# Optimization experiments

Measured on AMD Instinct MI355X. Metric: run time of the kernel, lower is better.

## Reference

```python
import jax, jax.numpy as jnp
import numpy as np

N, E, IN, HID, Z, H = 10000, 320000, 128, 128, 64, 4


def setup_inputs() -> dict:
    key = jax.random.key(0)
    ks = jax.random.split(key, 24)
    s = 0.05
    inp = {
        "x": jax.random.normal(ks[0], (N, IN), jnp.float32),
        "edge_index": jax.random.randint(ks[1], (2, E), 0, N, jnp.int32),
        "eps": jax.random.normal(ks[2], (N, Z), jnp.float32),
        # GCNConv params
        "gcn_w": jax.random.normal(ks[3], (IN, HID), jnp.float32) * s,
        "gcn_b": jnp.zeros((HID,), jnp.float32),
        # GATConv params (heads=H, out=HID per head, concat=False)
        "gat_w": jax.random.normal(ks[4], (HID, H * HID), jnp.float32) * s,
        "gat_att_src": jax.random.normal(ks[5], (H, HID), jnp.float32) * s,
        "gat_att_dst": jax.random.normal(ks[6], (H, HID), jnp.float32) * s,
        "gat_b": jnp.zeros((HID,), jnp.float32),
        # encoder MLP
        "mlp_w1": jax.random.normal(ks[7], (HID, HID), jnp.float32) * s,
        "mlp_b1": jnp.zeros((HID,), jnp.float32),
        "mlp_w2": jax.random.normal(ks[8], (HID, HID), jnp.float32) * s,
        "mlp_b2": jnp.zeros((HID,), jnp.float32),
        "mu_w": jax.random.normal(ks[9], (HID, Z), jnp.float32) * s,
        "mu_b": jnp.zeros((Z,), jnp.float32),
        "lv_w": jax.random.normal(ks[10], (HID, Z), jnp.float32) * s,
        "lv_b": jnp.zeros((Z,), jnp.float32),
        # decoder
        "dec_w1": jax.random.normal(ks[11], (Z, HID), jnp.float32) * s,
        "dec_b1": jnp.zeros((HID,), jnp.float32),
        "dec_w2": jax.random.normal(ks[12], (HID, Z), jnp.float32) * s,
        "dec_b2": jnp.zeros((Z,), jnp.float32),
    }
    return inp


def _forward(x, eps, gcn_w, gcn_b, gat_w, gat_att_src, gat_att_dst, gat_b,
             mlp_w1, mlp_b1, mlp_w2, mlp_b2, mu_w, mu_b, lv_w, lv_b,
             dec_w1, dec_b1, dec_w2, dec_b2, src, dst):
    n = x.shape[0]
    # ---- GCNConv (symmetric norm, self loops already in src/dst) ----
    h = x @ gcn_w  # [N, HID]
    deg = jax.ops.segment_sum(jnp.ones_like(dst, jnp.float32), dst, num_segments=n)
    dinv = jnp.where(deg > 0, deg ** -0.5, 0.0)
    msg = h[src] * (dinv[src] * dinv[dst])[:, None]  # [E', HID]
    h = jax.nn.relu(jax.ops.segment_sum(msg, dst, num_segments=n) + gcn_b)
    # ---- GATConv (heads=H, concat=False -> mean over heads) ----
    g = (h @ gat_w).reshape(n, H, HID)  # [N,H,D]
    a_src = jnp.einsum("nhd,hd->nh", g, gat_att_src)  # [N,H]
    a_dst = jnp.einsum("nhd,hd->nh", g, gat_att_dst)
    e = jax.nn.leaky_relu(a_src[src] + a_dst[dst], 0.2)  # [E',H]
    emax = jax.ops.segment_max(e, dst, num_segments=n)
    ex = jnp.exp(e - emax[dst])
    den = jax.ops.segment_sum(ex, dst, num_segments=n)
    alpha = ex / den[dst]  # softmax over incoming edges
    agg = jax.ops.segment_sum(alpha[:, :, None] * g[src], dst, num_segments=n)
    h = jax.nn.relu(agg.mean(axis=1) + gat_b)  # [N,HID]
    # ---- MLP ----
    h = jax.nn.relu(h @ mlp_w1 + mlp_b1)
    h = jax.nn.relu(h @ mlp_w2 + mlp_b2)
    mu = h @ mu_w + mu_b
    logvar = h @ lv_w + lv_b
    # ---- reparameterize ----
    lv = jnp.clip(logvar, -10.0, 10.0)
    z = mu + eps * jnp.exp(0.5 * lv)
    # ---- decoder ----
    d = jax.nn.relu(z @ dec_w1 + dec_b1)
    d = d @ dec_w2 + dec_b2 + z
    logits = d @ d.T  # [N,N]
    return logits, mu, logvar


def reference(x, edge_index, eps, gcn_w, gcn_b, gat_w, gat_att_src, gat_att_dst,
              gat_b, mlp_w1, mlp_b1, mlp_w2, mlp_b2, mu_w, mu_b, lv_w, lv_b,
              dec_w1, dec_b1, dec_w2, dec_b2):
    n = x.shape[0]
    loop = jnp.arange(n, dtype=edge_index.dtype)
    src = jnp.concatenate([edge_index[0], loop])
    dst = jnp.concatenate([edge_index[1], loop])
    return _forward(x, eps, gcn_w, gcn_b, gat_w, gat_att_src, gat_att_dst,
                    gat_b, mlp_w1, mlp_b1, mlp_w2, mlp_b2, mu_w, mu_b,
                    lv_w, lv_b, dec_w1, dec_b1, dec_w2, dec_b2, src, dst)
```

## Files before the change

kernel.cpp:

```cpp
#include <hip/hip_runtime.h>
#include <hip/hip_bf16.h>

typedef unsigned short u16;
typedef unsigned int u32;

#define NN 10000
#define EE 320000

typedef __attribute__((ext_vector_type(8))) short short8;
typedef __attribute__((ext_vector_type(4))) float f32x4;

__device__ __forceinline__ u16 f2bfu(float f) {
    u32 x = __float_as_uint(f);
    x += 0x7FFFu + ((x >> 16) & 1u);
    return (u16)(x >> 16);
}
__device__ __forceinline__ float bfu2f(u16 u) { return __uint_as_float(((u32)u) << 16); }
__device__ __forceinline__ void ld4f(const float* p, float* o) {
    float4 v = *(const float4*)p; o[0] = v.x; o[1] = v.y; o[2] = v.z; o[3] = v.w;
}

__global__ void k_hist(const int* __restrict__ dst, int* __restrict__ cnt) {
    int e = blockIdx.x * 256 + threadIdx.x;
    if (e < EE) atomicAdd(&cnt[dst[e]], 1);
}

__global__ void k_dinv(const int* __restrict__ cnt, float* __restrict__ dinv) {
    int n = blockIdx.x * 256 + threadIdx.x;
    if (n < NN) dinv[n] = 1.f / sqrtf((float)(cnt[n] + 1));
}

__global__ void k_scan(const int* __restrict__ cnt, int* __restrict__ rowptr) {
    __shared__ int sh[1024];
    int t = threadIdx.x;
    int base = t * 10;
    int loc[10];
    int s = 0;
    #pragma unroll
    for (int i = 0; i < 10; i++) {
        int idx = base + i;
        int v = (idx < NN) ? cnt[idx] : 0;
        loc[i] = s; s += v;
    }
    sh[t] = s;
    __syncthreads();
    for (int off = 1; off < 1024; off <<= 1) {
        int v = (t >= off) ? sh[t - off] : 0;
        __syncthreads();
        sh[t] += v;
        __syncthreads();
    }
    int ex = sh[t] - s;
    #pragma unroll
    for (int i = 0; i < 10; i++) {
        int idx = base + i;
        if (idx < NN) rowptr[idx] = ex + loc[i];
    }
    if (t == 0) rowptr[NN] = EE;
}

__global__ void k_scatter(const int* __restrict__ src, const int* __restrict__ dst,
                          const int* __restrict__ rowptr, int* __restrict__ fill,
                          int* __restrict__ csr) {
    int e = blockIdx.x * 256 + threadIdx.x;
    if (e < EE) {
        int d = dst[e];
        int pos = rowptr[d] + atomicAdd(&fill[d], 1);
        csr[pos] = src[e];
    }
}

template <int K, int M, bool RELU, bool BIAS, bool OB16>
__global__ __launch_bounds__(256) void k_linear(const float* __restrict__ A, const float* __restrict__ W,
                                                const float* __restrict__ Bb, void* __restrict__ outv) {
    constexpr int MC = M / 64;
    int wid = (blockIdx.x * blockDim.x + threadIdx.x) >> 6;
    int lane = threadIdx.x & 63;
    int row0 = wid * 4;
    if (row0 >= NN) return;
    float acc[4][MC];
    #pragma unroll
    for (int i = 0; i < 4; i++)
        #pragma unroll
        for (int j = 0; j < MC; j++) acc[i][j] = 0.f;
    for (int k = 0; k < K; k += 4) {
        float a[4][4];
        #pragma unroll
        for (int i = 0; i < 4; i++) ld4f(A + (size_t)(row0 + i) * K + k, a[i]);
        #pragma unroll
        for (int kk = 0; kk < 4; kk++) {
            float wv[MC];
            #pragma unroll
            for (int j = 0; j < MC; j++) wv[j] = W[(size_t)(k + kk) * M + j * 64 + lane];
            #pragma unroll
            for (int i = 0; i < 4; i++)
                #pragma unroll
                for (int j = 0; j < MC; j++) acc[i][j] += a[i][kk] * wv[j];
        }
    }
    float* outf = (float*)outv;
    u16*   outb = (u16*)outv;
    #pragma unroll
    for (int i = 0; i < 4; i++) {
        int r = row0 + i;
        #pragma unroll
        for (int j = 0; j < MC; j++) {
            float v = acc[i][j];
            if constexpr (BIAS) v += Bb[j * 64 + lane];
            if constexpr (RELU) v = fmaxf(v, 0.f);
            if constexpr (OB16) outb[(size_t)r * M + j * 64 + lane] = f2bfu(v);
            else                outf[(size_t)r * M + j * 64 + lane] = v;
        }
    }
}

__global__ __launch_bounds__(256) void k_gcn_agg(const u16* __restrict__ h0, const int* __restrict__ rowptr,
                                                 const int* __restrict__ csr, const float* __restrict__ dinv,
                                                 const float* __restrict__ bias, float* __restrict__ h1) {
    int node = (blockIdx.x * blockDim.x + threadIdx.x) >> 6;
    int lane = threadIdx.x & 63;
    if (node >= NN) return;
    float di = dinv[node];
    u32 sv = *(const u32*)(h0 + (size_t)node * 128 + lane * 2);
    float acc0 = bfu2f((u16)(sv & 0xffffu)) * di * di;
    float acc1 = bfu2f((u16)(sv >> 16)) * di * di;
    int st = rowptr[node], en = rowptr[node + 1];
    for (int p = st; p < en; p++) {
        int s = csr[p];
        float w = dinv[s] * di;
        u32 gv = *(const u32*)(h0 + (size_t)s * 128 + lane * 2);
        acc0 += bfu2f((u16)(gv & 0xffffu)) * w;
        acc1 += bfu2f((u16)(gv >> 16)) * w;
    }
    acc0 = fmaxf(acc0 + bias[lane * 2], 0.f);
    acc1 = fmaxf(acc1 + bias[lane * 2 + 1], 0.f);
    float2 o; o.x = acc0; o.y = acc1;
    *(float2*)(h1 + (size_t)node * 128 + lane * 2) = o;
}

__global__ __launch_bounds__(256) void k_gat_linear(const float* __restrict__ A, const float* __restrict__ W,
                                                    const float* __restrict__ att_s, const float* __restrict__ att_d,
                                                    u16* __restrict__ gbf, float* __restrict__ a_src,
                                                    float* __restrict__ a_dst) {
    int wid = (blockIdx.x * blockDim.x + threadIdx.x) >> 6;
    int lane = threadIdx.x & 63;
    int row0 = wid * 4;
    if (row0 >= NN) return;
    float acc[4][8];
    #pragma unroll
    for (int i = 0; i < 4; i++)
        #pragma unroll
        for (int t = 0; t < 8; t++) acc[i][t] = 0.f;
    for (int k = 0; k < 128; k += 4) {
        float a[4][4];
        #pragma unroll
        for (int i = 0; i < 4; i++) ld4f(A + (size_t)(row0 + i) * 128 + k, a[i]);
        #pragma unroll
        for (int kk = 0; kk < 4; kk++) {
            float wv[8];
            ld4f(W + (size_t)(k + kk) * 512 + lane * 8, wv);
            ld4f(W + (size_t)(k + kk) * 512 + lane * 8 + 4, wv + 4);
            #pragma unroll
            for (int i = 0; i < 4; i++)
                #pragma unroll
                for (int t = 0; t < 8; t++) acc[i][t] += a[i][kk] * wv[t];
        }
    }
    float sv[8], dv[8];
    ld4f(att_s + lane * 8, sv); ld4f(att_s + lane * 8 + 4, sv + 4);
    ld4f(att_d + lane * 8, dv); ld4f(att_d + lane * 8 + 4, dv + 4);
    int head = lane >> 4;
    #pragma unroll
    for (int i = 0; i < 4; i++) {
        int r = row0 + i;
        short8 pk;
        #pragma unroll
        for (int t = 0; t < 8; t++) pk[t] = (short)f2bfu(acc[i][t]);
        *(short8*)(gbf + (size_t)r * 512 + lane * 8) = pk;
        float ps = 0.f, pd = 0.f;
        #pragma unroll
        for (int t = 0; t < 8; t++) { ps += acc[i][t] * sv[t]; pd += acc[i][t] * dv[t]; }
        #pragma unroll
        for (int off = 1; off < 16; off <<= 1) {
            ps += __shfl_xor(ps, off, 64);
            pd += __shfl_xor(pd, off, 64);
        }
        if ((lane & 15) == i) {
            a_src[r * 4 + head] = ps;
            a_dst[r * 4 + head] = pd;
        }
    }
}

__global__ __launch_bounds__(256) void k_gat_softmax(const int* __restrict__ rowptr, const int* __restrict__ csr,
                                                     const float* __restrict__ a_src, const float* __restrict__ a_dst,
                                                     float* __restrict__ alpha, float* __restrict__ selfalpha) {
    int node = (blockIdx.x * blockDim.x + threadIdx.x) >> 6;
    int lane = threadIdx.x & 63;
    if (node >= NN) return;
    float ad[4], asn[4];
    ld4f(a_dst + node * 4, ad);
    ld4f(a_src + node * 4, asn);
    float es[4], m[4];
    #pragma unroll
    for (int h = 0; h < 4; h++) {
        float e = asn[h] + ad[h];
        es[h] = e > 0.f ? e : 0.2f * e;
        m[h] = es[h];
    }
    int st = rowptr[node], en = rowptr[node + 1];
    for (int p = st + lane; p < en; p += 64) {
        int s = csr[p];
        float as[4]; ld4f(a_src + s * 4, as);
        #pragma unroll
        for (int h = 0; h < 4; h++) {
            float e = as[h] + ad[h];
            e = e > 0.f ? e : 0.2f * e;
            m[h] = fmaxf(m[h], e);
        }
    }
    #pragma unroll
    for (int h = 0; h < 4; h++)
        for (int off = 1; off < 64; off <<= 1) m[h] = fmaxf(m[h], __shfl_xor(m[h], off, 64));
    float den[4];
    #pragma unroll
    for (int h = 0; h < 4; h++) den[h] = (lane == 0) ? __expf(es[h] - m[h]) : 0.f;
    for (int p = st + lane; p < en; p += 64) {
        int s = csr[p];
        float as[4]; ld4f(a_src + s * 4, as);
        #pragma unroll
        for (int h = 0; h < 4; h++) {
            float e = as[h] + ad[h];
            e = e > 0.f ? e : 0.2f * e;
            den[h] += __expf(e - m[h]);
        }
    }
    #pragma unroll
    for (int h = 0; h < 4; h++)
        for (int off = 1; off < 64; off <<= 1) den[h] += __shfl_xor(den[h], off, 64);
    float inv[4];
    #pragma unroll
    for (int h = 0; h < 4; h++) inv[h] = 1.f / den[h];
    for (int p = st + lane; p < en; p += 64) {
        int s = csr[p];
        float as[4]; ld4f(a_src + s * 4, as);
        float4 al;
        float av[4];
        #pragma unroll
        for (int h = 0; h < 4; h++) {
            float e = as[h] + ad[h];
            e = e > 0.f ? e : 0.2f * e;
            av[h] = __expf(e - m[h]) * inv[h];
        }
        al.x = av[0]; al.y = av[1]; al.z = av[2]; al.w = av[3];
        *(float4*)(alpha + (size_t)p * 4) = al;
    }
    if (lane == 0) {
        float4 sa;
        sa.x = __expf(es[0] - m[0]) * inv[0];
        sa.y = __expf(es[1] - m[1]) * inv[1];
        sa.z = __expf(es[2] - m[2]) * inv[2];
        sa.w = __expf(es[3] - m[3]) * inv[3];
        *(float4*)(selfalpha + (size_t)node * 4) = sa;
    }
}

__global__ __launch_bounds__(256) void k_gat_agg(const u16* __restrict__ gbf, const int* __restrict__ rowptr,
                                                 const int* __restrict__ csr, const float* __restrict__ alpha,
                                                 const float* __restrict__ selfalpha, const float* __restrict__ bias,
                                                 float* __restrict__ h2) {
    int node = (blockIdx.x * blockDim.x + threadIdx.x) >> 6;
    int lane = threadIdx.x & 63;
    if (node >= NN) return;
    int head = lane >> 4;
    float acc[8];
    float sa = selfalpha[(size_t)node * 4 + head];
    short8 gs = *(const short8*)(gbf + (size_t)node * 512 + lane * 8);
    #pragma unroll
    for (int t = 0; t < 8; t++) acc[t] = sa * bfu2f((u16)gs[t]);
    int st = rowptr[node], en = rowptr[node + 1];
    for (int p = st; p < en; p++) {
        int s = csr[p];
        float al = alpha[(size_t)p * 4 + head];
        short8 gv = *(const short8*)(gbf + (size_t)s * 512 + lane * 8);
        #pragma unroll
        for (int t = 0; t < 8; t++) acc[t] += al * bfu2f((u16)gv[t]);
    }
    #pragma unroll
    for (int t = 0; t < 8; t++) {
        acc[t] += __shfl_xor(acc[t], 16, 64);
        acc[t] += __shfl_xor(acc[t], 32, 64);
    }
    if (lane < 16) {
        int d0 = lane * 8;
        float o[8];
        #pragma unroll
        for (int t = 0; t < 8; t++) o[t] = fmaxf(acc[t] * 0.25f + bias[d0 + t], 0.f);
        float4 v0, v1;
        v0.x = o[0]; v0.y = o[1]; v0.z = o[2]; v0.w = o[3];
        v1.x = o[4]; v1.y = o[5]; v1.z = o[6]; v1.w = o[7];
        *(float4*)(h2 + (size_t)node * 128 + d0) = v0;
        *(float4*)(h2 + (size_t)node * 128 + d0 + 4) = v1;
    }
}

__global__ __launch_bounds__(256) void k_heads(const float* __restrict__ A, const float* __restrict__ muW,
                                               const float* __restrict__ muB, const float* __restrict__ lvW,
                                               const float* __restrict__ lvB, const float* __restrict__ eps,
                                               float* __restrict__ mu_out, float* __restrict__ lv_out,
                                               float* __restrict__ z) {
    int wid = (blockIdx.x * blockDim.x + threadIdx.x) >> 6;
    int lane = threadIdx.x & 63;
    int row0 = wid * 4;
    if (row0 >= NN) return;
    float am[4] = {0.f, 0.f, 0.f, 0.f};
    float av[4] = {0.f, 0.f, 0.f, 0.f};
    for (int k = 0; k < 128; k += 4) {
        float a[4][4];
        #pragma unroll
        for (int i = 0; i < 4; i++) ld4f(A + (size_t)(row0 + i) * 128 + k, a[i]);
        #pragma unroll
        for (int kk = 0; kk < 4; kk++) {
            float wm = muW[(k + kk) * 64 + lane];
            float wl = lvW[(k + kk) * 64 + lane];
            #pragma unroll
            for (int i = 0; i < 4; i++) { am[i] += a[i][kk] * wm; av[i] += a[i][kk] * wl; }
        }
    }
    float bm = muB[lane], bl = lvB[lane];
    #pragma unroll
    for (int i = 0; i < 4; i++) {
        size_t idx = (size_t)(row0 + i) * 64 + lane;
        float mu = am[i] + bm;
        float lv = av[i] + bl;
        mu_out[idx] = mu;
        lv_out[idx] = lv;
        float c = fminf(fmaxf(lv, -10.f), 10.f);
        z[idx] = mu + eps[idx] * __expf(0.5f * c);
    }
}

__global__ __launch_bounds__(256) void k_dec2(const float* __restrict__ A, const float* __restrict__ W,
                                              const float* __restrict__ Bb, const float* __restrict__ z,
                                              u16* __restrict__ dbf) {
    int wid = (blockIdx.x * blockDim.x + threadIdx.x) >> 6;
    int lane = threadIdx.x & 63;
    int row0 = wid * 4;
    if (row0 >= NN) return;
    float acc[4] = {0.f, 0.f, 0.f, 0.f};
    for (int k = 0; k < 128; k += 4) {
        float a[4][4];
        #pragma unroll
        for (int i = 0; i < 4; i++) ld4f(A + (size_t)(row0 + i) * 128 + k, a[i]);
        #pragma unroll
        for (int kk = 0; kk < 4; kk++) {
            float wv = W[(k + kk) * 64 + lane];
            #pragma unroll
            for (int i = 0; i < 4; i++) acc[i] += a[i][kk] * wv;
        }
    }
    float b = Bb[lane];
    #pragma unroll
    for (int i = 0; i < 4; i++) {
        size_t idx = (size_t)(row0 + i) * 64 + lane;
        dbf[idx] = f2bfu(acc[i] + b + z[idx]);
    }
}

__global__ __launch_bounds__(256) void k_logits(const u16* __restrict__ dbf, float* __restrict__ out) {
    __shared__ float tile[64][132];
    int tid = threadIdx.x;
    int wave = tid >> 6;
    int lane = tid & 63;
    int l15 = lane & 15, quad = lane >> 4;
    int rowhalf = wave >> 1;
    int i0 = blockIdx.y * 128 + rowhalf * 64;
    int j0 = blockIdx.x * 128 + (wave & 1) * 64;

    f32x4 acc[4][4];
    #pragma unroll
    for (int r = 0; r < 4; r++)
        #pragma unroll
        for (int c = 0; c < 4; c++) acc[r][c] = (f32x4){0.f, 0.f, 0.f, 0.f};

    #pragma unroll
    for (int ks = 0; ks < 64; ks += 32) {
        short8 a[4], b[4];
        #pragma unroll
        for (int r = 0; r < 4; r++) {
            int row = i0 + r * 16 + l15;
            if (row < NN) a[r] = *(const short8*)(dbf + (size_t)row * 64 + ks + quad * 8);
            else a[r] = (short8){0, 0, 0, 0, 0, 0, 0, 0};
        }
        #pragma unroll
        for (int c = 0; c < 4; c++) {
            int row = j0 + c * 16 + l15;
            if (row < NN) b[c] = *(const short8*)(dbf + (size_t)row * 64 + ks + quad * 8);
            else b[c] = (short8){0, 0, 0, 0, 0, 0, 0, 0};
        }
        #pragma unroll
        for (int r = 0; r < 4; r++)
            #pragma unroll
            for (int c = 0; c < 4; c++)
                acc[r][c] = __builtin_amdgcn_mfma_f32_16x16x32_bf16(a[r], b[c], acc[r][c], 0, 0, 0);
    }

    int lc0 = (wave & 1) * 64;
    #pragma unroll
    for (int chunk = 0; chunk < 2; chunk++) {
        if (rowhalf == chunk) {
            #pragma unroll
            for (int r = 0; r < 4; r++)
                #pragma unroll
                for (int c = 0; c < 4; c++)
                    #pragma unroll
                    for (int v = 0; v < 4; v++)
                        tile[r * 16 + quad * 4 + v][lc0 + c * 16 + l15] = acc[r][c][v];
        }
        __syncthreads();
        #pragma unroll
        for (int it = 0; it < 8; it++) {
            int idx = it * 256 + tid;
            int row = idx >> 5, ch = idx & 31;
            int rg = blockIdx.y * 128 + chunk * 64 + row;
            int cg = blockIdx.x * 128 + ch * 4;
            if (rg < NN && cg < NN) {
                f32x4 v = *(const f32x4*)&tile[row][ch * 4];
                __builtin_nontemporal_store(v, (f32x4*)(out + (size_t)rg * NN + cg));
            }
        }
        __syncthreads();
    }
}

extern "C" void kernel_launch(void* const* d_in, const int* in_sizes, int n_in,
                              void* d_out, int out_size, void* d_ws, size_t ws_size,
                              hipStream_t stream) {
    const float* x      = (const float*)d_in[0];
    const int*   ei     = (const int*)d_in[1];
    const float* eps    = (const float*)d_in[2];
    const float* gcn_w  = (const float*)d_in[3];
    const float* gcn_b  = (const float*)d_in[4];
    const float* gat_w  = (const float*)d_in[5];
    const float* att_s  = (const float*)d_in[6];
    const float* att_d  = (const float*)d_in[7];
    const float* gat_b  = (const float*)d_in[8];
    const float* mlp_w1 = (const float*)d_in[9];
    const float* mlp_b1 = (const float*)d_in[10];
    const float* mlp_w2 = (const float*)d_in[11];
    const float* mlp_b2 = (const float*)d_in[12];
    const float* mu_w   = (const float*)d_in[13];
    const float* mu_b   = (const float*)d_in[14];
    const float* lv_w   = (const float*)d_in[15];
    const float* lv_b   = (const float*)d_in[16];
    const float* dec_w1 = (const float*)d_in[17];
    const float* dec_b1 = (const float*)d_in[18];
    const float* dec_w2 = (const float*)d_in[19];
    const float* dec_b2 = (const float*)d_in[20];

    float* out    = (float*)d_out;
    float* out_mu = out + (size_t)NN * NN;
    float* out_lv = out_mu + (size_t)NN * 64;

    char* ws = (char*)d_ws;
    size_t off = 0;
    auto alloc = [&](size_t bytes) -> void* {
        void* p = ws + off;
        off += (bytes + 255) & ~(size_t)255;
        return p;
    };
    int*   cnt       = (int*)alloc(NN * 4);
    int*   fill      = (int*)alloc(NN * 4);
    int*   rowptr    = (int*)alloc((NN + 1) * 4);
    int*   csr       = (int*)alloc(EE * 4);
    float* dinv      = (float*)alloc(NN * 4);
    float* a_src     = (float*)alloc(NN * 4 * 4);
    float* a_dst     = (float*)alloc(NN * 4 * 4);
    float* selfalpha = (float*)alloc(NN * 4 * 4);
    float* z         = (float*)alloc((size_t)NN * 64 * 4);
    float* h2        = (float*)alloc((size_t)NN * 128 * 4);
    float* bufA      = (float*)alloc((size_t)NN * 128 * 4);
    float* bufB      = (float*)alloc((size_t)NN * 128 * 4);
    float* bufC      = (float*)alloc((size_t)NN * 512 * 4);
    float* bufD      = (float*)alloc((size_t)EE * 4 * 4);

    u16*   h0bf  = (u16*)bufA;
    float* h1    = bufB;
    u16*   gbf   = (u16*)bufC;
    float* alpha = bufD;
    float* m1    = bufA;
    float* m2    = bufB;
    float* t1    = bufC;
    u16*   dbf   = (u16*)bufD;

    const int* src = ei;
    const int* dst = ei + EE;

    hipMemsetAsync(cnt, 0, NN * 4, stream);
    hipMemsetAsync(fill, 0, NN * 4, stream);

    k_hist<<<(EE + 255) / 256, 256, 0, stream>>>(dst, cnt);
    k_dinv<<<(NN + 255) / 256, 256, 0, stream>>>(cnt, dinv);
    k_scan<<<1, 1024, 0, stream>>>(cnt, rowptr);
    k_scatter<<<(EE + 255) / 256, 256, 0, stream>>>(src, dst, rowptr, fill, csr);

    k_linear<128, 128, false, false, true><<<625, 256, 0, stream>>>(x, gcn_w, nullptr, h0bf);
    k_gcn_agg<<<2500, 256, 0, stream>>>(h0bf, rowptr, csr, dinv, gcn_b, h1);

    k_gat_linear<<<625, 256, 0, stream>>>(h1, gat_w, att_s, att_d, gbf, a_src, a_dst);
    k_gat_softmax<<<2500, 256, 0, stream>>>(rowptr, csr, a_src, a_dst, alpha, selfalpha);
    k_gat_agg<<<2500, 256, 0, stream>>>(gbf, rowptr, csr, alpha, selfalpha, gat_b, h2);

    k_linear<128, 128, true, true, false><<<625, 256, 0, stream>>>(h2, mlp_w1, mlp_b1, m1);
    k_linear<128, 128, true, true, false><<<625, 256, 0, stream>>>(m1, mlp_w2, mlp_b2, m2);
    k_heads<<<625, 256, 0, stream>>>(m2, mu_w, mu_b, lv_w, lv_b, eps, out_mu, out_lv, z);

    k_linear<64, 128, true, true, false><<<625, 256, 0, stream>>>(z, dec_w1, dec_b1, t1);
    k_dec2<<<625, 256, 0, stream>>>(t1, dec_w2, dec_b2, z, dbf);

    dim3 lgrid((NN + 127) / 128, (NN + 127) / 128);
    k_logits<<<lgrid, 256, 0, stream>>>(dbf, out);
}
```

Before: 760.8 us.

## Fuse GAT softmax into aggregation and merge MLP/decoder chains into single kernels

Folds the dinv computation into the scan kernel. Replaces the separate GAT softmax and aggregation kernels with one kernel that takes a per-head max, then accumulates unnormalized exp weights and the denominator in the same pass, so no per-edge alpha array is written or read. The two MLP layers and the mu/logvar heads now run in one kernel, as do the two decoder layers, with intermediates kept in shared memory instead of global buffers. This cuts kernel launches and global round trips, at the cost of the exp being recomputed redundantly across the 16 lanes of each head inside the serial edge loop.

```diff
diff --git a/kernel.cpp b/kernel.cpp
--- a/kernel.cpp
+++ b/kernel.cpp
@@ -25,21 +25,18 @@
     if (e < EE) atomicAdd(&cnt[dst[e]], 1);
 }
 
-__global__ void k_dinv(const int* __restrict__ cnt, float* __restrict__ dinv) {
-    int n = blockIdx.x * 256 + threadIdx.x;
-    if (n < NN) dinv[n] = 1.f / sqrtf((float)(cnt[n] + 1));
-}
-
-__global__ void k_scan(const int* __restrict__ cnt, int* __restrict__ rowptr) {
+__global__ void k_scan(const int* __restrict__ cnt, int* __restrict__ rowptr,
+                       float* __restrict__ dinv) {
     __shared__ int sh[1024];
     int t = threadIdx.x;
     int base = t * 10;
-    int loc[10];
+    int loc[10], cv[10];
     int s = 0;
     #pragma unroll
     for (int i = 0; i < 10; i++) {
         int idx = base + i;
         int v = (idx < NN) ? cnt[idx] : 0;
+        cv[i] = v;
         loc[i] = s; s += v;
     }
     sh[t] = s;
@@ -54,7 +51,10 @@
     #pragma unroll
     for (int i = 0; i < 10; i++) {
         int idx = base + i;
-        if (idx < NN) rowptr[idx] = ex + loc[i];
+        if (idx < NN) {
+            rowptr[idx] = ex + loc[i];
+            dinv[idx] = 1.f / sqrtf((float)(cv[i] + 1));
+        }
     }
     if (t == 0) rowptr[NN] = EE;
 }
@@ -192,100 +192,45 @@
     }
 }
 
-__global__ __launch_bounds__(256) void k_gat_softmax(const int* __restrict__ rowptr, const int* __restrict__ csr,
-                                                     const float* __restrict__ a_src, const float* __restrict__ a_dst,
-                                                     float* __restrict__ alpha, float* __restrict__ selfalpha) {
+__global__ __launch_bounds__(256) void k_gat_sa(const u16* __restrict__ gbf, const int* __restrict__ rowptr,
+                                                const int* __restrict__ csr, const float* __restrict__ a_src,
+                                                const float* __restrict__ a_dst, const float* __restrict__ bias,
+                                                float* __restrict__ h2) {
     int node = (blockIdx.x * blockDim.x + threadIdx.x) >> 6;
     int lane = threadIdx.x & 63;
     if (node >= NN) return;
-    float ad[4], asn[4];
-    ld4f(a_dst + node * 4, ad);
-    ld4f(a_src + node * 4, asn);
-    float es[4], m[4];
-    #pragma unroll
-    for (int h = 0; h < 4; h++) {
-        float e = asn[h] + ad[h];
-        es[h] = e > 0.f ? e : 0.2f * e;
-        m[h] = es[h];
-    }
+    int head = lane >> 4, l15 = lane & 15;
+    float ad = a_dst[node * 4 + head];
+    float es = a_src[node * 4 + head] + ad;
+    es = es > 0.f ? es : 0.2f * es;
+    float m = es;
     int st = rowptr[node], en = rowptr[node + 1];
-    for (int p = st + lane; p < en; p += 64) {
-        int s = csr[p];
-        float as[4]; ld4f(a_src + s * 4, as);
-        #pragma unroll
-        for (int h = 0; h < 4; h++) {
-            float e = as[h] + ad[h];
-            e = e > 0.f ? e : 0.2f * e;
-            m[h] = fmaxf(m[h], e);
-        }
-    }
-    #pragma unroll
-    for (int h = 0; h < 4; h++)
-        for (int off = 1; off < 64; off <<= 1) m[h] = fmaxf(m[h], __shfl_xor(m[h], off, 64));
-    float den[4];
-    #pragma unroll
-    for (int h = 0; h < 4; h++) den[h] = (lane == 0) ? __expf(es[h] - m[h]) : 0.f;
-    for (int p = st + lane; p < en; p += 64) {
-        int s = csr[p];
-        float as[4]; ld4f(a_src + s * 4, as);
-        #pragma unroll
-        for (int h = 0; h < 4; h++) {
-            float e = as[h] + ad[h];
-            e = e > 0.f ? e : 0.2f * e;
-            den[h] += __expf(e - m[h]);
-        }
-    }
-    #pragma unroll
-    for (int h = 0; h < 4; h++)
-        for (int off = 1; off < 64; off <<= 1) den[h] += __shfl_xor(den[h], off, 64);
-    float inv[4];
-    #pragma unroll
-    for (int h = 0; h < 4; h++) inv[h] = 1.f / den[h];
-    for (int p = st + lane; p < en; p += 64) {
-        int s = csr[p];
-        float as[4]; ld4f(a_src + s * 4, as);
-        float4 al;
-        float av[4];
-        #pragma unroll
-        for (int h = 0; h < 4; h++) {
-            float e = as[h] + ad[h];
-            e = e > 0.f ? e : 0.2f * e;
-            av[h] = __expf(e - m[h]) * inv[h];
-        }
-        al.x = av[0]; al.y = av[1]; al.z = av[2]; al.w = av[3];
-        *(float4*)(alpha + (size_t)p * 4) = al;
-    }
-    if (lane == 0) {
-        float4 sa;
-        sa.x = __expf(es[0] - m[0]) * inv[0];
-        sa.y = __expf(es[1] - m[1]) * inv[1];
-        sa.z = __expf(es[2] - m[2]) * inv[2];
-        sa.w = __expf(es[3] - m[3]) * inv[3];
-        *(float4*)(selfalpha + (size_t)node * 4) = sa;
-    }
-}
-
-__global__ __launch_bounds__(256) void k_gat_agg(const u16* __restrict__ gbf, const int* __restrict__ rowptr,
-                                                 const int* __restrict__ csr, const float* __restrict__ alpha,
-                                                 const float* __restrict__ selfalpha, const float* __restrict__ bias,
-                                                 float* __restrict__ h2) {
-    int node = (blockIdx.x * blockDim.x + threadIdx.x) >> 6;
-    int lane = threadIdx.x & 63;
-    if (node >= NN) return;
-    int head = lane >> 4;
+    for (int p = st + l15; p < en; p += 16) {
+        float e = a_src[csr[p] * 4 + head] + ad;
+        e = e > 0.f ? e : 0.2f * e;
+        m = fmaxf(m, e);
+    }
+    #pragma unroll
+    for (int off = 1; off < 16; off <<= 1) m = fmaxf(m, __shfl_xor(m, off, 64));
+    float w0 = __expf(es - m);
+    float den = w0;
     float acc[8];
-    float sa = selfalpha[(size_t)node * 4 + head];
     short8 gs = *(const short8*)(gbf + (size_t)node * 512 + lane * 8);
     #pragma unroll
-    for (int t = 0; t < 8; t++) acc[t] = sa * bfu2f((u16)gs[t]);
-    int st = rowptr[node], en = rowptr[node + 1];
+    for (int t = 0; t < 8; t++) acc[t] = w0 * bfu2f((u16)gs[t]);
     for (int p = st; p < en; p++) {
         int s = csr[p];
-        float al = alpha[(size_t)p * 4 + head];
+        float e = a_src[s * 4 + head] + ad;
+        e = e > 0.f ? e : 0.2f * e;
+        float w = __expf(e - m);
+        den += w;
         short8 gv = *(const short8*)(gbf + (size_t)s * 512 + lane * 8);
         #pragma unroll
-        for (int t = 0; t < 8; t++) acc[t] += al * bfu2f((u16)gv[t]);
-    }
+        for (int t = 0; t < 8; t++) acc[t] += w * bfu2f((u16)gv[t]);
+    }
+    float inv = 1.f / den;
+    #pragma unroll
+    for (int t = 0; t < 8; t++) acc[t] *= inv;
     #pragma unroll
     for (int t = 0; t < 8; t++) {
         acc[t] += __shfl_xor(acc[t], 16, 64);
@@ -304,21 +249,63 @@
     }
 }
 
-__global__ __launch_bounds__(256) void k_heads(const float* __restrict__ A, const float* __restrict__ muW,
-                                               const float* __restrict__ muB, const float* __restrict__ lvW,
-                                               const float* __restrict__ lvB, const float* __restrict__ eps,
-                                               float* __restrict__ mu_out, float* __restrict__ lv_out,
-                                               float* __restrict__ z) {
-    int wid = (blockIdx.x * blockDim.x + threadIdx.x) >> 6;
+__global__ __launch_bounds__(256) void k_mlp(const float* __restrict__ A,
+                                             const float* __restrict__ W1, const float* __restrict__ B1,
+                                             const float* __restrict__ W2, const float* __restrict__ B2,
+                                             const float* __restrict__ muW, const float* __restrict__ muB,
+                                             const float* __restrict__ lvW, const float* __restrict__ lvB,
+                                             const float* __restrict__ eps, float* __restrict__ mu_out,
+                                             float* __restrict__ lv_out, float* __restrict__ z) {
+    __shared__ float t[4][4][128];
+    int wave = threadIdx.x >> 6;
     int lane = threadIdx.x & 63;
-    int row0 = wid * 4;
-    if (row0 >= NN) return;
+    int row0 = blockIdx.x * 16 + wave * 4;
+    float acc[4][2];
+    #pragma unroll
+    for (int i = 0; i < 4; i++) { acc[i][0] = 0.f; acc[i][1] = 0.f; }
+    for (int k = 0; k < 128; k += 4) {
+        float a[4][4];
+        #pragma unroll
+        for (int i = 0; i < 4; i++) ld4f(A + (size_t)(row0 + i) * 128 + k, a[i]);
+        #pragma unroll
+        for (int kk = 0; kk < 4; kk++) {
+            float w0 = W1[(size_t)(k + kk) * 128 + lane];
+            float w1 = W1[(size_t)(k + kk) * 128 + 64 + lane];
+            #pragma unroll
+            for (int i = 0; i < 4; i++) { acc[i][0] += a[i][kk] * w0; acc[i][1] += a[i][kk] * w1; }
+        }
+    }
+    #pragma unroll
+    for (int i = 0; i < 4; i++) {
+        t[wave][i][lane]      = fmaxf(acc[i][0] + B1[lane], 0.f);
+        t[wave][i][64 + lane] = fmaxf(acc[i][1] + B1[64 + lane], 0.f);
+    }
+    float acc2[4][2];
+    #pragma unroll
+    for (int i = 0; i < 4; i++) { acc2[i][0] = 0.f; acc2[i][1] = 0.f; }
+    for (int k = 0; k < 128; k += 4) {
+        float a[4][4];
+        #pragma unroll
+        for (int i = 0; i < 4; i++) ld4f(&t[wave][i][k], a[i]);
+        #pragma unroll
+        for (int kk = 0; kk < 4; kk++) {
+            float w0 = W2[(size_t)(k + kk) * 128 + lane];
+            float w1 = W2[(size_t)(k + kk) * 128 + 64 + lane];
+            #pragma unroll
+            for (int i = 0; i < 4; i++) { acc2[i][0] += a[i][kk] * w0; acc2[i][1] += a[i][kk] * w1; }
+        }
+    }
+    #pragma unroll
+    for (int i = 0; i < 4; i++) {
+        t[wave][i][lane]      = fmaxf(acc2[i][0] + B2[lane], 0.f);
+        t[wave][i][64 + lane] = fmaxf(acc2[i][1] + B2[64 + lane], 0.f);
+    }
     float am[4] = {0.f, 0.f, 0.f, 0.f};
     float av[4] = {0.f, 0.f, 0.f, 0.f};
     for (int k = 0; k < 128; k += 4) {
         float a[4][4];
         #pragma unroll
-        for (int i = 0; i < 4; i++) ld4f(A + (size_t)(row0 + i) * 128 + k, a[i]);
+        for (int i = 0; i < 4; i++) ld4f(&t[wave][i][k], a[i]);
         #pragma unroll
         for (int kk = 0; kk < 4; kk++) {
             float wm = muW[(k + kk) * 64 + lane];
@@ -340,30 +327,51 @@
     }
 }
 
-__global__ __launch_bounds__(256) void k_dec2(const float* __restrict__ A, const float* __restrict__ W,
-                                              const float* __restrict__ Bb, const float* __restrict__ z,
-                                              u16* __restrict__ dbf) {
-    int wid = (blockIdx.x * blockDim.x + threadIdx.x) >> 6;
+__global__ __launch_bounds__(256) void k_dec(const float* __restrict__ z,
+                                             const float* __restrict__ W1, const float* __restrict__ B1,
+                                             const float* __restrict__ W2, const float* __restrict__ B2,
+                                             u16* __restrict__ dbf) {
+    __shared__ float t[4][4][128];
+    int wave = threadIdx.x >> 6;
     int lane = threadIdx.x & 63;
-    int row0 = wid * 4;
-    if (row0 >= NN) return;
-    float acc[4] = {0.f, 0.f, 0.f, 0.f};
+    int row0 = blockIdx.x * 16 + wave * 4;
+    float acc[4][2];
+    #pragma unroll
+    for (int i = 0; i < 4; i++) { acc[i][0] = 0.f; acc[i][1] = 0.f; }
+    for (int k = 0; k < 64; k += 4) {
+        float a[4][4];
+        #pragma unroll
+        for (int i = 0; i < 4; i++) ld4f(z + (size_t)(row0 + i) * 64 + k, a[i]);
+        #pragma unroll
+        for (int kk = 0; kk < 4; kk++) {
+            float w0 = W1[(size_t)(k + kk) * 128 + lane];
+            float w1 = W1[(size_t)(k + kk) * 128 + 64 + lane];
+            #pragma unroll
+            for (int i = 0; i < 4; i++) { acc[i][0] += a[i][kk] * w0; acc[i][1] += a[i][kk] * w1; }
+        }
+    }
+    #pragma unroll
+    for (int i = 0; i < 4; i++) {
+        t[wave][i][lane]      = fmaxf(acc[i][0] + B1[lane], 0.f);
+        t[wave][i][64 + lane] = fmaxf(acc[i][1] + B1[64 + lane], 0.f);
+    }
+    float acc2[4] = {0.f, 0.f, 0.f, 0.f};
     for (int k = 0; k < 128; k += 4) {
         float a[4][4];
         #pragma unroll
-        for (int i = 0; i < 4; i++) ld4f(A + (size_t)(row0 + i) * 128 + k, a[i]);
-        #pragma unroll
-        for (int kk = 0; kk < 4; kk++) {
-            float wv = W[(k + kk) * 64 + lane];
-            #pragma unroll
-            for (int i = 0; i < 4; i++) acc[i] += a[i][kk] * wv;
-        }
-    }
-    float b = Bb[lane];
+        for (int i = 0; i < 4; i++) ld4f(&t[wave][i][k], a[i]);
+        #pragma unroll
+        for (int kk = 0; kk < 4; kk++) {
+            float wv = W2[(size_t)(k + kk) * 64 + lane];
+            #pragma unroll
+            for (int i = 0; i < 4; i++) acc2[i] += a[i][kk] * wv;
+        }
+    }
+    float b = B2[lane];
     #pragma unroll
     for (int i = 0; i < 4; i++) {
         size_t idx = (size_t)(row0 + i) * 64 + lane;
-        dbf[idx] = f2bfu(acc[i] + b + z[idx]);
+        dbf[idx] = f2bfu(acc2[i] + b + z[idx]);
     }
 }
 
@@ -469,29 +477,24 @@
         off += (bytes + 255) & ~(size_t)255;
         return p;
     };
-    int*   cnt       = (int*)alloc(NN * 4);
-    int*   fill      = (int*)alloc(NN * 4);
-    int*   rowptr    = (int*)alloc((NN + 1) * 4);
-    int*   csr       = (int*)alloc(EE * 4);
-    float* dinv      = (float*)alloc(NN * 4);
-    float* a_src     = (float*)alloc(NN * 4 * 4);
-    float* a_dst     = (float*)alloc(NN * 4 * 4);
-    float* selfalpha = (float*)alloc(NN * 4 * 4);
-    float* z         = (float*)alloc((size_t)NN * 64 * 4);
-    float* h2        = (float*)alloc((size_t)NN * 128 * 4);
-    float* bufA      = (float*)alloc((size_t)NN * 128 * 4);
-    float* bufB      = (float*)alloc((size_t)NN * 128 * 4);
-    float* bufC      = (float*)alloc((size_t)NN * 512 * 4);
-    float* bufD      = (float*)alloc((size_t)EE * 4 * 4);
-
-    u16*   h0bf  = (u16*)bufA;
-    float* h1    = bufB;
-    u16*   gbf   = (u16*)bufC;
-    float* alpha = bufD;
-    float* m1    = bufA;
-    float* m2    = bufB;
-    float* t1    = bufC;
-    u16*   dbf   = (u16*)bufD;
+    int*   cnt    = (int*)alloc(NN * 4);
+    int*   fill   = (int*)alloc(NN * 4);
+    int*   rowptr = (int*)alloc((NN + 1) * 4);
+    int*   csr    = (int*)alloc(EE * 4);
+    float* dinv   = (float*)alloc(NN * 4);
+    float* a_src  = (float*)alloc(NN * 4 * 4);
+    float* a_dst  = (float*)alloc(NN * 4 * 4);
+    float* z      = (float*)alloc((size_t)NN * 64 * 4);
+    float* h2     = (float*)alloc((size_t)NN * 128 * 4);
+    float* bufA   = (float*)alloc((size_t)NN * 128 * 4);
+    float* bufB   = (float*)alloc((size_t)NN * 128 * 4);
+    float* bufC   = (float*)alloc((size_t)NN * 512 * 4);
+    float* bufD   = (float*)alloc((size_t)NN * 64 * 2);
+
+    u16*   h0bf = (u16*)bufA;
+    float* h1   = bufB;
+    u16*   gbf  = (u16*)bufC;
+    u16*   dbf  = (u16*)bufD;
 
     const int* src = ei;
     const int* dst = ei + EE;
@@ -500,23 +503,19 @@
     hipMemsetAsync(fill, 0, NN * 4, stream);
 
     k_hist<<<(EE + 255) / 256, 256, 0, stream>>>(dst, cnt);
-    k_dinv<<<(NN + 255) / 256, 256, 0, stream>>>(cnt, dinv);
-    k_scan<<<1, 1024, 0, stream>>>(cnt, rowptr);
+    k_scan<<<1, 1024, 0, stream>>>(cnt, rowptr, dinv);
     k_scatter<<<(EE + 255) / 256, 256, 0, stream>>>(src, dst, rowptr, fill, csr);
 
     k_linear<128, 128, false, false, true><<<625, 256, 0, stream>>>(x, gcn_w, nullptr, h0bf);
     k_gcn_agg<<<2500, 256, 0, stream>>>(h0bf, rowptr, csr, dinv, gcn_b, h1);
 
     k_gat_linear<<<625, 256, 0, stream>>>(h1, gat_w, att_s, att_d, gbf, a_src, a_dst);
-    k_gat_softmax<<<2500, 256, 0, stream>>>(rowptr, csr, a_src, a_dst, alpha, selfalpha);
-    k_gat_agg<<<2500, 256, 0, stream>>>(gbf, rowptr, csr, alpha, selfalpha, gat_b, h2);
-
-    k_linear<128, 128, true, true, false><<<625, 256, 0, stream>>>(h2, mlp_w1, mlp_b1, m1);
-    k_linear<128, 128, true, true, false><<<625, 256, 0, stream>>>(m1, mlp_w2, mlp_b2, m2);
-    k_heads<<<625, 256, 0, stream>>>(m2, mu_w, mu_b, lv_w, lv_b, eps, out_mu, out_lv, z);
-
-    k_linear<64, 128, true, true, false><<<625, 256, 0, stream>>>(z, dec_w1, dec_b1, t1);
-    k_dec2<<<625, 256, 0, stream>>>(t1, dec_w2, dec_b2, z, dbf);
+    k_gat_sa<<<2500, 256, 0, stream>>>(gbf, rowptr, csr, a_src, a_dst, gat_b, h2);
+
+    k_mlp<<<625, 256, 0, stream>>>(h2, mlp_w1, mlp_b1, mlp_w2, mlp_b2,
+                                   mu_w, mu_b, lv_w, lv_b, eps, out_mu, out_lv, z);
+
+    k_dec<<<625, 256, 0, stream>>>(z, dec_w1, dec_b1, dec_w2, dec_b2, dbf);
 
     dim3 lgrid((NN + 127) / 128, (NN + 127) / 128);
     k_logits<<<lgrid, 256, 0, stream>>>(dbf, out);
```

After: 721.4 us. -5.2%, faster.
